# Kernel optimization log

Measured on AMD Instinct MI355X. Metric: run time of the kernel, lower is better.

Reference implementation:

```python
import jax, jax.numpy as jnp
import numpy as np

N = 10000
E = 160000
UNITS = 64
NUM_RBF = 32
CUTOFF = 1.0


def _xavier(k, shape):
    fan_out, fan_in = shape
    lim = float(np.sqrt(6.0 / (fan_in + fan_out)))
    return jax.random.uniform(k, shape, minval=-lim, maxval=lim, dtype=jnp.float32)


def setup_inputs() -> dict:
    key = jax.random.key(0)
    ks = jax.random.split(key, 16)
    inp = {
        "edge_index": jax.random.randint(ks[0], (2, E), 0, N),
        "edge_weight": jax.random.uniform(ks[1], (E,), dtype=jnp.float32),
        "edge_attr": jax.random.normal(ks[2], (E, NUM_RBF), dtype=jnp.float32),
        "X": jax.random.normal(ks[3], (N, UNITS, 3, 3), dtype=jnp.float32),
        # scalar MLP: num_rbf -> units -> 2*units -> 3*units
        "Ws0": _xavier(ks[4], (UNITS, NUM_RBF)), "bs0": jnp.zeros((UNITS,), jnp.float32),
        "Ws1": _xavier(ks[5], (2 * UNITS, UNITS)), "bs1": jnp.zeros((2 * UNITS,), jnp.float32),
        "Ws2": _xavier(ks[6], (3 * UNITS, 2 * UNITS)), "bs2": jnp.zeros((3 * UNITS,), jnp.float32),
    }
    for i in range(6):
        inp[f"Wt{i}"] = _xavier(ks[7 + i], (UNITS, UNITS))
    return inp


def cosine_cutoff(r, cutoff):
    return jnp.where(r < cutoff, 0.5 * (jnp.cos(jnp.pi * r / cutoff) + 1.0), 0.0)


def tensor_norm(X):
    # X: [N, units, 3, 3] -> [N, units]
    return jnp.sum(X * X, axis=(-2, -1))


def decompose_tensor(X):
    eye = jnp.eye(3, dtype=X.dtype)
    trace = jnp.trace(X, axis1=-2, axis2=-1)  # [N, units]
    I = (trace / 3.0)[..., None, None] * eye
    A = 0.5 * (X - jnp.swapaxes(X, -2, -1))
    S = 0.5 * (X + jnp.swapaxes(X, -2, -1)) - I
    return I, A, S


def channel_linear(T, W):
    # linear over the channel dim: [N, c, 3, 3] x [d, c] -> [N, d, 3, 3]
    return jnp.einsum('ncij,dc->ndij', T, W)


def reference(edge_index, edge_weight, edge_attr, X,
              Ws0, bs0, Ws1, bs1, Ws2, bs2,
              Wt0, Wt1, Wt2, Wt3, Wt4, Wt5):
    act = jax.nn.silu
    C = cosine_cutoff(edge_weight, CUTOFF)  # [E]
    h = act(edge_attr @ Ws0.T + bs0)
    h = act(h @ Ws1.T + bs1)
    h = act(h @ Ws2.T + bs2)  # [E, 3*units]
    ea = (h * C[:, None]).reshape(h.shape[0], UNITS, 3)  # [E, units, 3]

    X = X / (tensor_norm(X) + 1.0)[..., None, None]
    I, A, S = decompose_tensor(X)
    I = channel_linear(I, Wt0)
    A = channel_linear(A, Wt1)
    S = channel_linear(S, Wt2)
    Y = I + A + S

    src, dst = edge_index[0], edge_index[1]
    n = X.shape[0]
    # message = per-edge radial scaling of gathered node tensors; aggregate at src
    Im = jax.ops.segment_sum(ea[..., 0, None, None] * I[dst], src, num_segments=n)
    Am = jax.ops.segment_sum(ea[..., 1, None, None] * A[dst], src, num_segments=n)
    Sm = jax.ops.segment_sum(ea[..., 2, None, None] * S[dst], src, num_segments=n)
    msg = Im + Am + Sm

    # O(3): symmetrized product of batched 3x3 matmuls
    AB = jnp.matmul(msg, Y) + jnp.matmul(Y, msg)
    I2, A2, S2 = decompose_tensor(AB)
    normp1 = (tensor_norm(I2 + A2 + S2) + 1.0)[..., None, None]
    I2 = channel_linear(I2 / normp1, Wt3)
    A2 = channel_linear(A2 / normp1, Wt4)
    S2 = channel_linear(S2 / normp1, Wt5)
    dX = I2 + A2 + S2
    return X + dX + jnp.matmul(dX, dX)
```

## Files before the change

### kernel.cpp

```cpp
#include <hip/hip_runtime.h>
#include <math.h>

#define NN 10000
#define EE 160000

#define OFF_WTT 0
#define OFF_PK  24576
#define OFF_B2P 41984
#define OFF_IASH 42176
#define OFF_EAH 3242176
#define OFF_ATTRP 18602176
#define OFF_CP  21162176
#define OFF_INT 21322176

typedef __attribute__((ext_vector_type(8))) _Float16 h16x8;
typedef __attribute__((ext_vector_type(2))) __fp16 fp16x2_raw;
typedef __attribute__((ext_vector_type(4))) float f32x4;

__device__ __forceinline__ float silu_f(float x) {
    return x * __builtin_amdgcn_rcpf(1.0f + __expf(-x));
}
__device__ __forceinline__ unsigned int pkh(float a, float b) {
    union { fp16x2_raw h; unsigned int u; } cv;
    cv.h = __builtin_amdgcn_cvt_pkrtz(a, b);
    return cv.u;
}
__device__ __forceinline__ unsigned short f2h(float f) {
    union { _Float16 h; unsigned short u; } cv; cv.h = (_Float16)f; return cv.u;
}
__device__ __forceinline__ float h2f(unsigned short s) {
    union { unsigned short u; _Float16 h; } cv; cv.u = s; return (float)cv.h;
}
__device__ __forceinline__ float h2f_lo(unsigned int u) { return h2f((unsigned short)(u & 0xffffu)); }
__device__ __forceinline__ float h2f_hi(unsigned int u) { return h2f((unsigned short)(u >> 16)); }

__global__ void k_prep(const float* __restrict__ Wt0, const float* __restrict__ Wt1,
                       const float* __restrict__ Wt2, const float* __restrict__ Wt3,
                       const float* __restrict__ Wt4, const float* __restrict__ Wt5,
                       const float* __restrict__ Ws0, const float* __restrict__ Ws1,
                       const float* __restrict__ Ws2, const float* __restrict__ bs2,
                       const int* __restrict__ ei,
                       float* __restrict__ WtT, unsigned short* __restrict__ PK,
                       float* __restrict__ bs2p, int* __restrict__ counts) {
    int idx = blockIdx.x * 256 + threadIdx.x;
    if (idx < 24576) {
        int k = idx >> 12, r = idx & 4095;
        int c = r >> 6, d = r & 63;
        const float* W = (k == 0) ? Wt0 : (k == 1) ? Wt1 : (k == 2) ? Wt2
                       : (k == 3) ? Wt3 : (k == 4) ? Wt4 : Wt5;
        WtT[idx] = W[d * 64 + c];
    } else if (idx < 26624) {
        int q = idx - 24576;
        int ot = q >> 9, r = q & 511, lane = r >> 3, j = r & 7;
        int k = ((lane >> 4) * 8) + j, o = ot * 16 + (lane & 15);
        PK[q] = f2h(Ws0[o * 32 + k]);
    } else if (idx < 34816) {
        int q = idx - 24576;
        int i = q - 2048, ch = i >> 9, r = i & 511, lane = r >> 3, j = r & 7;
        int ot = ch >> 1, ks = ch & 1;
        int k = ks * 32 + (lane >> 4) * 8 + j, o = ot * 16 + (lane & 15);
        PK[q] = f2h(Ws1[o * 64 + k]);
    } else if (idx < 59392) {
        int q = idx - 24576;
        int i = q - 10240, ch = i >> 9, r = i & 511, lane = r >> 3, j = r & 7;
        int ot = ch >> 2, ks = ch & 3;
        int k = ks * 32 + (lane >> 4) * 8 + j;
        int op = ot * 16 + (lane & 15);
        int o = (op & 63) * 3 + (op >> 6);
        PK[q] = f2h(Ws2[o * 128 + k]);
    } else if (idx < 59584) {
        int op = idx - 59392;
        bs2p[op] = bs2[(op & 63) * 3 + (op >> 6)];
    } else if (idx < 59584 + EE) {
        int e = idx - 59584;
        atomicAdd(&counts[ei[e]], 1);
    }
}

__global__ __launch_bounds__(256) void k_scan(const int* __restrict__ counts,
                                              int* __restrict__ offsets) {
    __shared__ int sums[256];
    int t = threadIdx.x;
    int base = t * 40;
    int s = 0;
    if (base < NN) {
        const int4* p = (const int4*)(counts + base);
#pragma unroll
        for (int q = 0; q < 10; ++q) { int4 a = p[q]; s += a.x + a.y + a.z + a.w; }
    }
    sums[t] = s;
    __syncthreads();
    for (int off = 1; off < 256; off <<= 1) {
        int tmp = (t >= off) ? sums[t - off] : 0;
        __syncthreads();
        sums[t] += tmp;
        __syncthreads();
    }
    int run = sums[t] - s;
    if (base < NN) {
        const int4* p = (const int4*)(counts + base);
#pragma unroll
        for (int q = 0; q < 10; ++q) {
            int4 a = p[q];
            offsets[base + 4 * q + 0] = run; run += a.x;
            offsets[base + 4 * q + 1] = run; run += a.y;
            offsets[base + 4 * q + 2] = run; run += a.z;
            offsets[base + 4 * q + 3] = run; run += a.w;
        }
    }
    if (t == 255) offsets[NN] = run;
}

__global__ void k_fill(const int* __restrict__ ei, const int* __restrict__ offsets,
                       const float* __restrict__ attr, const float* __restrict__ ew,
                       int* __restrict__ cursor, int* __restrict__ dstp,
                       unsigned short* __restrict__ attrP, float* __restrict__ Cp) {
    int e = blockIdx.x * 256 + threadIdx.x;
    if (e < EE) {
        int s = ei[e];
        int pos = offsets[s] + atomicAdd(&cursor[s], 1);
        dstp[pos] = ei[EE + e];
        const float4* ap = (const float4*)(attr + (size_t)e * 32);
        unsigned int pk[16];
#pragma unroll
        for (int q = 0; q < 8; ++q) {
            float4 v = ap[q];
            pk[2 * q]     = pkh(v.x, v.y);
            pk[2 * q + 1] = pkh(v.z, v.w);
        }
        uint4* dst = (uint4*)(attrP + (size_t)pos * 32);
#pragma unroll
        for (int q = 0; q < 4; ++q)
            dst[q] = make_uint4(pk[4 * q], pk[4 * q + 1], pk[4 * q + 2], pk[4 * q + 3]);
        float rw = ew[e];
        Cp[pos] = (rw < 1.0f) ? 0.5f * (cosf(3.14159265358979f * rw) + 1.0f) : 0.0f;
    }
}

__global__ __launch_bounds__(256) void k_mlpnp(const unsigned short* __restrict__ attrP,
                                               const float* __restrict__ Cp,
                                               const unsigned short* __restrict__ PK,
                                               const float* __restrict__ bs0,
                                               const float* __restrict__ bs1,
                                               const float* __restrict__ bs2p,
                                               const float* __restrict__ X,
                                               const float* __restrict__ WtT,
                                               unsigned short* __restrict__ eah,
                                               unsigned int* __restrict__ IASu) {
    __shared__ unsigned short SH[4][4352];
    int t = threadIdx.x, w = t >> 6, l = t & 63;
    if (blockIdx.x < EE / 128) {
        int lr = l & 15, lg = l >> 4;
        int base = blockIdx.x * 128 + w * 32;
        unsigned short* Hh = SH[w];
        const h16x8* P1 = (const h16x8*)PK;
        const h16x8* P2 = (const h16x8*)(PK + 2048);
        const h16x8* P3 = (const h16x8*)(PK + 10240);
        union { h16x8 h; uint4 v; } B1[2];
        float C[2];
#pragma unroll
        for (int tt = 0; tt < 2; ++tt) {
            int p = base + tt * 16 + lr;
            B1[tt].v = *((const uint4*)(attrP + (size_t)p * 32) + lg);
            C[tt] = Cp[p];
        }
#pragma unroll
        for (int ot = 0; ot < 4; ++ot) {
            h16x8 wf = P1[ot * 64 + l];
            float4 bb = *(const float4*)&bs0[ot * 16 + lg * 4];
#pragma unroll
            for (int tt = 0; tt < 2; ++tt) {
                f32x4 acc = {bb.x, bb.y, bb.z, bb.w};
                acc = __builtin_amdgcn_mfma_f32_16x16x32_f16(wf, B1[tt].h, acc, 0, 0, 0);
                unsigned int u01 = pkh(silu_f(acc[0]), silu_f(acc[1]));
                unsigned int u23 = pkh(silu_f(acc[2]), silu_f(acc[3]));
                *(uint2*)&Hh[tt * 2176 + lr * 136 + ot * 16 + lg * 4] = make_uint2(u01, u23);
            }
        }
        __builtin_amdgcn_wave_barrier();
        h16x8 B2a[2], B2b[2];
#pragma unroll
        for (int tt = 0; tt < 2; ++tt) {
            B2a[tt] = *(const h16x8*)&Hh[tt * 2176 + lr * 136 + lg * 8];
            B2b[tt] = *(const h16x8*)&Hh[tt * 2176 + lr * 136 + 32 + lg * 8];
        }
        __builtin_amdgcn_wave_barrier();
#pragma unroll
        for (int ot = 0; ot < 8; ++ot) {
            h16x8 wf0 = P2[(ot * 2 + 0) * 64 + l];
            h16x8 wf1 = P2[(ot * 2 + 1) * 64 + l];
            float4 bb = *(const float4*)&bs1[ot * 16 + lg * 4];
#pragma unroll
            for (int tt = 0; tt < 2; ++tt) {
                f32x4 acc = {bb.x, bb.y, bb.z, bb.w};
                acc = __builtin_amdgcn_mfma_f32_16x16x32_f16(wf0, B2a[tt], acc, 0, 0, 0);
                acc = __builtin_amdgcn_mfma_f32_16x16x32_f16(wf1, B2b[tt], acc, 0, 0, 0);
                unsigned int u01 = pkh(silu_f(acc[0]), silu_f(acc[1]));
                unsigned int u23 = pkh(silu_f(acc[2]), silu_f(acc[3]));
                *(uint2*)&Hh[tt * 2176 + lr * 136 + ot * 16 + lg * 4] = make_uint2(u01, u23);
            }
        }
        __builtin_amdgcn_wave_barrier();
        h16x8 B3[4][2];
#pragma unroll
        for (int ks = 0; ks < 4; ++ks)
#pragma unroll
            for (int tt = 0; tt < 2; ++tt)
                B3[ks][tt] = *(const h16x8*)&Hh[tt * 2176 + lr * 136 + ks * 32 + lg * 8];
#pragma unroll
        for (int ot = 0; ot < 12; ++ot) {
            h16x8 wf0 = P3[(ot * 4 + 0) * 64 + l];
            h16x8 wf1 = P3[(ot * 4 + 1) * 64 + l];
            h16x8 wf2 = P3[(ot * 4 + 2) * 64 + l];
            h16x8 wf3 = P3[(ot * 4 + 3) * 64 + l];
            float4 bb = *(const float4*)&bs2p[ot * 16 + lg * 4];
#pragma unroll
            for (int tt = 0; tt < 2; ++tt) {
                f32x4 acc = {bb.x, bb.y, bb.z, bb.w};
                acc = __builtin_amdgcn_mfma_f32_16x16x32_f16(wf0, B3[0][tt], acc, 0, 0, 0);
                acc = __builtin_amdgcn_mfma_f32_16x16x32_f16(wf1, B3[1][tt], acc, 0, 0, 0);
                acc = __builtin_amdgcn_mfma_f32_16x16x32_f16(wf2, B3[2][tt], acc, 0, 0, 0);
                acc = __builtin_amdgcn_mfma_f32_16x16x32_f16(wf3, B3[3][tt], acc, 0, 0, 0);
                unsigned int u01 = pkh(silu_f(acc[0]) * C[tt], silu_f(acc[1]) * C[tt]);
                unsigned int u23 = pkh(silu_f(acc[2]) * C[tt], silu_f(acc[3]) * C[tt]);
                *(uint2*)&eah[(size_t)(base + tt * 16 + lr) * 192 + ot * 16 + lg * 4]
                    = make_uint2(u01, u23);
            }
        }
    } else {
        int c = l;
        int n = (blockIdx.x - EE / 128) * 4 + w;
        float* xs = (float*)SH[w];
        float (*L12)[12] = (float (*)[12])(xs + 576);
#pragma unroll
        for (int i = 0; i < 9; i++) xs[c + 64 * i] = X[(size_t)n * 576 + c + 64 * i];
        __builtin_amdgcn_wave_barrier();
        float x[9];
#pragma unroll
        for (int j = 0; j < 9; j++) x[j] = xs[c * 9 + j];
        float nrm = 0.f;
#pragma unroll
        for (int j = 0; j < 9; j++) nrm += x[j] * x[j];
        float inv = __builtin_amdgcn_rcpf(nrm + 1.0f);
#pragma unroll
        for (int j = 0; j < 9; j++) x[j] *= inv;
        float tr3 = (x[0] + x[4] + x[8]) * (1.0f / 3.0f);
        L12[c][0] = tr3;
        L12[c][1] = 0.5f * (x[1] - x[3]);
        L12[c][2] = 0.5f * (x[2] - x[6]);
        L12[c][3] = 0.5f * (x[5] - x[7]);
        L12[c][4] = x[0] - tr3;
        L12[c][5] = x[4] - tr3;
        L12[c][6] = 0.5f * (x[1] + x[3]);
        L12[c][7] = 0.5f * (x[2] + x[6]);
        L12[c][8] = 0.5f * (x[5] + x[7]);
        __builtin_amdgcn_wave_barrier();
        int d = c;
        const float* W0 = WtT;
        const float* W1 = WtT + 4096;
        const float* W2 = WtT + 8192;
        float aI = 0, aA0 = 0, aA1 = 0, aA2 = 0, aS0 = 0, aS1 = 0, aS2 = 0, aS3 = 0, aS4 = 0;
        for (int cc = 0; cc < 64; ++cc) {
            float w0 = W0[cc * 64 + d], w1 = W1[cc * 64 + d], w2 = W2[cc * 64 + d];
            float4 L0 = *(const float4*)&L12[cc][0];
            float4 L1 = *(const float4*)&L12[cc][4];
            float L8 = L12[cc][8];
            aI  += w0 * L0.x;
            aA0 += w1 * L0.y; aA1 += w1 * L0.z; aA2 += w1 * L0.w;
            aS0 += w2 * L1.x; aS1 += w2 * L1.y; aS2 += w2 * L1.z;
            aS3 += w2 * L1.w; aS4 += w2 * L8;
        }
        unsigned int* op = IASu + (size_t)n * 320 + d;
        op[0]   = pkh(aI, aA0);
        op[64]  = pkh(aA1, aA2);
        op[128] = pkh(aS0, aS1);
        op[192] = pkh(aS2, aS3);
        op[256] = pkh(aS4, 0.0f);
    }
}

__global__ __launch_bounds__(256) void k_aggout(const int* __restrict__ offsets,
                                                const int* __restrict__ dstp,
                                                const unsigned short* __restrict__ eah,
                                                const unsigned int* __restrict__ IASu,
                                                const float* __restrict__ X,
                                                const float* __restrict__ WtT,
                                                float* __restrict__ out) {
    int t = threadIdx.x, w = t >> 6, c = t & 63;
    int n = blockIdx.x * 4 + w;
    __shared__ float XS[4][576];
    __shared__ float LO[4][768];
    float* xs = XS[w];
    float* lo = LO[w];
#pragma unroll
    for (int i = 0; i < 9; i++) xs[c + 64 * i] = X[(size_t)n * 576 + c + 64 * i];

    int beg = offsets[n], end = offsets[n + 1];
    float m0 = 0, m1 = 0, m2 = 0, m3 = 0, m4 = 0, m5 = 0, m6 = 0, m7 = 0, m8 = 0;
    int i = beg;
    for (; i + 4 <= end; i += 4) {
        float a[4][3];
        unsigned int u[4][5];
#pragma unroll
        for (int q = 0; q < 4; ++q) {
            const unsigned short* ep = eah + (size_t)(i + q) * 192;
            a[q][0] = h2f(ep[c]); a[q][1] = h2f(ep[64 + c]); a[q][2] = h2f(ep[128 + c]);
            const unsigned int* p = IASu + (size_t)dstp[i + q] * 320 + c;
            u[q][0] = p[0]; u[q][1] = p[64]; u[q][2] = p[128]; u[q][3] = p[192]; u[q][4] = p[256];
        }
#pragma unroll
        for (int q = 0; q < 4; ++q) {
            m0 += a[q][0] * h2f_lo(u[q][0]); m1 += a[q][1] * h2f_hi(u[q][0]);
            m2 += a[q][1] * h2f_lo(u[q][1]); m3 += a[q][1] * h2f_hi(u[q][1]);
            m4 += a[q][2] * h2f_lo(u[q][2]); m5 += a[q][2] * h2f_hi(u[q][2]);
            m6 += a[q][2] * h2f_lo(u[q][3]); m7 += a[q][2] * h2f_hi(u[q][3]);
            m8 += a[q][2] * h2f_lo(u[q][4]);
        }
    }
    for (; i < end; ++i) {
        const unsigned short* ep = eah + (size_t)i * 192;
        float a0 = h2f(ep[c]), a1 = h2f(ep[64 + c]), a2 = h2f(ep[128 + c]);
        const unsigned int* p = IASu + (size_t)dstp[i] * 320 + c;
        unsigned int u0 = p[0], u1 = p[64], u2 = p[128], u3 = p[192], u4 = p[256];
        m0 += a0 * h2f_lo(u0); m1 += a1 * h2f_hi(u0);
        m2 += a1 * h2f_lo(u1); m3 += a1 * h2f_hi(u1);
        m4 += a2 * h2f_lo(u2); m5 += a2 * h2f_hi(u2);
        m6 += a2 * h2f_lo(u3); m7 += a2 * h2f_hi(u3);
        m8 += a2 * h2f_lo(u4);
    }
    const unsigned int* yp = IASu + (size_t)n * 320 + c;
    unsigned int y0 = yp[0], y1 = yp[64], y2 = yp[128], y3 = yp[192], y4 = yp[256];
    float yI = h2f_lo(y0), yA0 = h2f_hi(y0), yA1 = h2f_lo(y1), yA2 = h2f_hi(y1);
    float yS0 = h2f_lo(y2), yS1 = h2f_hi(y2), yS2 = h2f_lo(y3), yS3 = h2f_hi(y3);
    float yS4 = h2f_lo(y4);

    float M[3][3] = {
        { m0 + m4,   m1 + m6,  m2 + m7 },
        { -m1 + m6,  m0 + m5,  m3 + m8 },
        { -m2 + m7, -m3 + m8,  m0 - m4 - m5 } };
    float Y[3][3] = {
        { yI + yS0,   yA0 + yS2,  yA1 + yS3 },
        { -yA0 + yS2, yI + yS1,   yA2 + yS4 },
        { -yA1 + yS3, -yA2 + yS4, yI - yS0 - yS1 } };
    float AB[3][3];
#pragma unroll
    for (int ii = 0; ii < 3; ii++)
#pragma unroll
        for (int j = 0; j < 3; j++) {
            float s = 0.f;
#pragma unroll
            for (int k = 0; k < 3; k++) s += M[ii][k] * Y[k][j] + Y[ii][k] * M[k][j];
            AB[ii][j] = s;
        }
    float tr3 = (AB[0][0] + AB[1][1] + AB[2][2]) * (1.0f / 3.0f);
    float fro = 0.f;
#pragma unroll
    for (int ii = 0; ii < 3; ii++)
#pragma unroll
        for (int j = 0; j < 3; j++) fro += AB[ii][j] * AB[ii][j];
    float inv = __builtin_amdgcn_rcpf(fro + 1.0f);
    float (*L12)[12] = (float (*)[12])lo;
    L12[c][0] = tr3 * inv;
    L12[c][1] = 0.5f * (AB[0][1] - AB[1][0]) * inv;
    L12[c][2] = 0.5f * (AB[0][2] - AB[2][0]) * inv;
    L12[c][3] = 0.5f * (AB[1][2] - AB[2][1]) * inv;
    L12[c][4] = (AB[0][0] - tr3) * inv;
    L12[c][5] = (AB[1][1] - tr3) * inv;
    L12[c][6] = 0.5f * (AB[0][1] + AB[1][0]) * inv;
    L12[c][7] = 0.5f * (AB[0][2] + AB[2][0]) * inv;
    L12[c][8] = 0.5f * (AB[1][2] + AB[2][1]) * inv;
    __builtin_amdgcn_wave_barrier();
    int d = c;
    const float* W3 = WtT + 3 * 4096;
    const float* W4 = WtT + 4 * 4096;
    const float* W5 = WtT + 5 * 4096;
    float aI = 0, aA0 = 0, aA1 = 0, aA2 = 0, aS0 = 0, aS1 = 0, aS2 = 0, aS3 = 0, aS4 = 0;
    for (int cc = 0; cc < 64; ++cc) {
        float w3 = W3[cc * 64 + d], w4 = W4[cc * 64 + d], w5 = W5[cc * 64 + d];
        float4 L0 = *(const float4*)&L12[cc][0];
        float4 L1 = *(const float4*)&L12[cc][4];
        float L8 = L12[cc][8];
        aI  += w3 * L0.x;
        aA0 += w4 * L0.y; aA1 += w4 * L0.z; aA2 += w4 * L0.w;
        aS0 += w5 * L1.x; aS1 += w5 * L1.y; aS2 += w5 * L1.z;
        aS3 += w5 * L1.w; aS4 += w5 * L8;
    }
    float dX[3][3] = {
        { aI + aS0,   aA0 + aS2,  aA1 + aS3 },
        { -aA0 + aS2, aI + aS1,   aA2 + aS4 },
        { -aA1 + aS3, -aA2 + aS4, aI - aS0 - aS1 } };
    float D2[3][3];
#pragma unroll
    for (int ii = 0; ii < 3; ii++)
#pragma unroll
        for (int j = 0; j < 3; j++) {
            float s = 0.f;
#pragma unroll
            for (int k = 0; k < 3; k++) s += dX[ii][k] * dX[k][j];
            D2[ii][j] = s;
        }
    float x[9];
    __builtin_amdgcn_wave_barrier();
#pragma unroll
    for (int j = 0; j < 9; j++) x[j] = xs[d * 9 + j];
    float nrm = 0.f;
#pragma unroll
    for (int j = 0; j < 9; j++) nrm += x[j] * x[j];
    float xinv = __builtin_amdgcn_rcpf(nrm + 1.0f);
    __builtin_amdgcn_wave_barrier();
#pragma unroll
    for (int ii = 0; ii < 3; ii++)
#pragma unroll
        for (int j = 0; j < 3; j++)
            lo[d * 9 + ii * 3 + j] = x[ii * 3 + j] * xinv + dX[ii][j] + D2[ii][j];
    __builtin_amdgcn_wave_barrier();
#pragma unroll
    for (int ii = 0; ii < 9; ii++) out[(size_t)n * 576 + c + 64 * ii] = lo[c + 64 * ii];
}

extern "C" void kernel_launch(void* const* d_in, const int* in_sizes, int n_in,
                              void* d_out, int out_size, void* d_ws, size_t ws_size,
                              hipStream_t stream) {
    (void)in_sizes; (void)n_in; (void)out_size; (void)ws_size;
    const int* ei = (const int*)d_in[0];
    const float* ew = (const float*)d_in[1];
    const float* attr = (const float*)d_in[2];
    const float* X = (const float*)d_in[3];
    const float* Ws0 = (const float*)d_in[4];
    const float* bs0 = (const float*)d_in[5];
    const float* Ws1 = (const float*)d_in[6];
    const float* bs1 = (const float*)d_in[7];
    const float* Ws2 = (const float*)d_in[8];
    const float* bs2 = (const float*)d_in[9];
    const float* Wt0 = (const float*)d_in[10];
    const float* Wt1 = (const float*)d_in[11];
    const float* Wt2 = (const float*)d_in[12];
    const float* Wt3 = (const float*)d_in[13];
    const float* Wt4 = (const float*)d_in[14];
    const float* Wt5 = (const float*)d_in[15];
    float* ws = (float*)d_ws;
    int* ibase = (int*)(ws + OFF_INT);
    int* counts = ibase;
    int* cursor = ibase + NN;
    int* offsets = ibase + 2 * NN;
    int* dstp = ibase + 3 * NN + 1;
    unsigned short* PK = (unsigned short*)(ws + OFF_PK);
    unsigned int* IASu = (unsigned int*)(ws + OFF_IASH);
    unsigned short* eah = (unsigned short*)(ws + OFF_EAH);
    unsigned short* attrP = (unsigned short*)(ws + OFF_ATTRP);
    float* Cp = ws + OFF_CP;

    (void)hipMemsetAsync(counts, 0, 2 * NN * sizeof(int), stream);
    k_prep<<<(59584 + EE + 255) / 256, 256, 0, stream>>>(
        Wt0, Wt1, Wt2, Wt3, Wt4, Wt5, Ws0, Ws1, Ws2, bs2, ei,
        ws, PK, ws + OFF_B2P, counts);
    k_scan<<<1, 256, 0, stream>>>(counts, offsets);
    k_fill<<<(EE + 255) / 256, 256, 0, stream>>>(ei, offsets, attr, ew, cursor, dstp, attrP, Cp);
    k_mlpnp<<<EE / 128 + NN / 4, 256, 0, stream>>>(attrP, Cp, PK, bs0, bs1, ws + OFF_B2P,
                                                   X, ws, eah, IASu);
    k_aggout<<<NN / 4, 256, 0, stream>>>(offsets, dstp, eah, IASu, X, ws, (float*)d_out);
}
```

Baseline: 150.3 us.

## Split fused MLP/node kernel and pass MLP activations via ds_bpermute instead of LDS

The combined edge-MLP and node-prep kernel is split into two launches: k_nodeprep for the per-node decomposition and channel linear, and k_mlp for the edge MLP. k_mlp now handles 16 edges per wave instead of 32 and drops the shared staging buffer. Hidden activations are rearranged between MFMA layers with cross-lane ds_bpermute shuffles and selects. This removes LDS use and pressure from the MLP so more waves can be resident, at the cost of an extra kernel launch, more permute instructions, and weight fragments reloaded per 16-edge tile instead of per 32-edge tile.

```diff
diff --git a/kernel.cpp b/kernel.cpp
--- a/kernel.cpp
+++ b/kernel.cpp
@@ -33,6 +33,9 @@
 }
 __device__ __forceinline__ float h2f_lo(unsigned int u) { return h2f((unsigned short)(u & 0xffffu)); }
 __device__ __forceinline__ float h2f_hi(unsigned int u) { return h2f((unsigned short)(u >> 16)); }
+__device__ __forceinline__ unsigned int bperm(int addr, unsigned int v) {
+    return (unsigned int)__builtin_amdgcn_ds_bpermute(addr, (int)v);
+}
 
 __global__ void k_prep(const float* __restrict__ Wt0, const float* __restrict__ Wt1,
                        const float* __restrict__ Wt2, const float* __restrict__ Wt3,
@@ -137,145 +140,132 @@
     }
 }
 
-__global__ __launch_bounds__(256) void k_mlpnp(const unsigned short* __restrict__ attrP,
-                                               const float* __restrict__ Cp,
-                                               const unsigned short* __restrict__ PK,
-                                               const float* __restrict__ bs0,
-                                               const float* __restrict__ bs1,
-                                               const float* __restrict__ bs2p,
-                                               const float* __restrict__ X,
-                                               const float* __restrict__ WtT,
-                                               unsigned short* __restrict__ eah,
-                                               unsigned int* __restrict__ IASu) {
-    __shared__ unsigned short SH[4][4352];
+__global__ __launch_bounds__(256) void k_nodeprep(const float* __restrict__ X,
+                                                  const float* __restrict__ WtT,
+                                                  unsigned int* __restrict__ IASu) {
+    int t = threadIdx.x, w = t >> 6, c = t & 63;
+    int n = blockIdx.x * 4 + w;
+    __shared__ float XS[4][576];
+    __shared__ float L[4][64][12];
+    float* xs = XS[w];
+#pragma unroll
+    for (int i = 0; i < 9; i++) xs[c + 64 * i] = X[(size_t)n * 576 + c + 64 * i];
+    __builtin_amdgcn_wave_barrier();
+    float x[9];
+#pragma unroll
+    for (int j = 0; j < 9; j++) x[j] = xs[c * 9 + j];
+    float nrm = 0.f;
+#pragma unroll
+    for (int j = 0; j < 9; j++) nrm += x[j] * x[j];
+    float inv = __builtin_amdgcn_rcpf(nrm + 1.0f);
+#pragma unroll
+    for (int j = 0; j < 9; j++) x[j] *= inv;
+    float tr3 = (x[0] + x[4] + x[8]) * (1.0f / 3.0f);
+    L[w][c][0] = tr3;
+    L[w][c][1] = 0.5f * (x[1] - x[3]);
+    L[w][c][2] = 0.5f * (x[2] - x[6]);
+    L[w][c][3] = 0.5f * (x[5] - x[7]);
+    L[w][c][4] = x[0] - tr3;
+    L[w][c][5] = x[4] - tr3;
+    L[w][c][6] = 0.5f * (x[1] + x[3]);
+    L[w][c][7] = 0.5f * (x[2] + x[6]);
+    L[w][c][8] = 0.5f * (x[5] + x[7]);
+    __builtin_amdgcn_wave_barrier();
+    int d = c;
+    const float* W0 = WtT;
+    const float* W1 = WtT + 4096;
+    const float* W2 = WtT + 8192;
+    float aI = 0, aA0 = 0, aA1 = 0, aA2 = 0, aS0 = 0, aS1 = 0, aS2 = 0, aS3 = 0, aS4 = 0;
+    for (int cc = 0; cc < 64; ++cc) {
+        float w0 = W0[cc * 64 + d], w1 = W1[cc * 64 + d], w2 = W2[cc * 64 + d];
+        float4 L0 = *(const float4*)&L[w][cc][0];
+        float4 L1 = *(const float4*)&L[w][cc][4];
+        float L8 = L[w][cc][8];
+        aI  += w0 * L0.x;
+        aA0 += w1 * L0.y; aA1 += w1 * L0.z; aA2 += w1 * L0.w;
+        aS0 += w2 * L1.x; aS1 += w2 * L1.y; aS2 += w2 * L1.z;
+        aS3 += w2 * L1.w; aS4 += w2 * L8;
+    }
+    unsigned int* op = IASu + (size_t)n * 320 + d;
+    op[0]   = pkh(aI, aA0);
+    op[64]  = pkh(aA1, aA2);
+    op[128] = pkh(aS0, aS1);
+    op[192] = pkh(aS2, aS3);
+    op[256] = pkh(aS4, 0.0f);
+}
+
+__global__ __launch_bounds__(256) void k_mlp(const unsigned short* __restrict__ attrP,
+                                             const float* __restrict__ Cp,
+                                             const unsigned short* __restrict__ PK,
+                                             const float* __restrict__ bs0,
+                                             const float* __restrict__ bs1,
+                                             const float* __restrict__ bs2p,
+                                             unsigned short* __restrict__ eah) {
     int t = threadIdx.x, w = t >> 6, l = t & 63;
-    if (blockIdx.x < EE / 128) {
-        int lr = l & 15, lg = l >> 4;
-        int base = blockIdx.x * 128 + w * 32;
-        unsigned short* Hh = SH[w];
-        const h16x8* P1 = (const h16x8*)PK;
-        const h16x8* P2 = (const h16x8*)(PK + 2048);
-        const h16x8* P3 = (const h16x8*)(PK + 10240);
-        union { h16x8 h; uint4 v; } B1[2];
-        float C[2];
-#pragma unroll
-        for (int tt = 0; tt < 2; ++tt) {
-            int p = base + tt * 16 + lr;
-            B1[tt].v = *((const uint4*)(attrP + (size_t)p * 32) + lg);
-            C[tt] = Cp[p];
-        }
-#pragma unroll
-        for (int ot = 0; ot < 4; ++ot) {
-            h16x8 wf = P1[ot * 64 + l];
-            float4 bb = *(const float4*)&bs0[ot * 16 + lg * 4];
-#pragma unroll
-            for (int tt = 0; tt < 2; ++tt) {
-                f32x4 acc = {bb.x, bb.y, bb.z, bb.w};
-                acc = __builtin_amdgcn_mfma_f32_16x16x32_f16(wf, B1[tt].h, acc, 0, 0, 0);
-                unsigned int u01 = pkh(silu_f(acc[0]), silu_f(acc[1]));
-                unsigned int u23 = pkh(silu_f(acc[2]), silu_f(acc[3]));
-                *(uint2*)&Hh[tt * 2176 + lr * 136 + ot * 16 + lg * 4] = make_uint2(u01, u23);
-            }
-        }
-        __builtin_amdgcn_wave_barrier();
-        h16x8 B2a[2], B2b[2];
-#pragma unroll
-        for (int tt = 0; tt < 2; ++tt) {
-            B2a[tt] = *(const h16x8*)&Hh[tt * 2176 + lr * 136 + lg * 8];
-            B2b[tt] = *(const h16x8*)&Hh[tt * 2176 + lr * 136 + 32 + lg * 8];
-        }
-        __builtin_amdgcn_wave_barrier();
-#pragma unroll
-        for (int ot = 0; ot < 8; ++ot) {
-            h16x8 wf0 = P2[(ot * 2 + 0) * 64 + l];
-            h16x8 wf1 = P2[(ot * 2 + 1) * 64 + l];
-            float4 bb = *(const float4*)&bs1[ot * 16 + lg * 4];
-#pragma unroll
-            for (int tt = 0; tt < 2; ++tt) {
-                f32x4 acc = {bb.x, bb.y, bb.z, bb.w};
-                acc = __builtin_amdgcn_mfma_f32_16x16x32_f16(wf0, B2a[tt], acc, 0, 0, 0);
-                acc = __builtin_amdgcn_mfma_f32_16x16x32_f16(wf1, B2b[tt], acc, 0, 0, 0);
-                unsigned int u01 = pkh(silu_f(acc[0]), silu_f(acc[1]));
-                unsigned int u23 = pkh(silu_f(acc[2]), silu_f(acc[3]));
-                *(uint2*)&Hh[tt * 2176 + lr * 136 + ot * 16 + lg * 4] = make_uint2(u01, u23);
-            }
-        }
-        __builtin_amdgcn_wave_barrier();
-        h16x8 B3[4][2];
-#pragma unroll
-        for (int ks = 0; ks < 4; ++ks)
-#pragma unroll
-            for (int tt = 0; tt < 2; ++tt)
-                B3[ks][tt] = *(const h16x8*)&Hh[tt * 2176 + lr * 136 + ks * 32 + lg * 8];
-#pragma unroll
-        for (int ot = 0; ot < 12; ++ot) {
-            h16x8 wf0 = P3[(ot * 4 + 0) * 64 + l];
-            h16x8 wf1 = P3[(ot * 4 + 1) * 64 + l];
-            h16x8 wf2 = P3[(ot * 4 + 2) * 64 + l];
-            h16x8 wf3 = P3[(ot * 4 + 3) * 64 + l];
-            float4 bb = *(const float4*)&bs2p[ot * 16 + lg * 4];
-#pragma unroll
-            for (int tt = 0; tt < 2; ++tt) {
-                f32x4 acc = {bb.x, bb.y, bb.z, bb.w};
-                acc = __builtin_amdgcn_mfma_f32_16x16x32_f16(wf0, B3[0][tt], acc, 0, 0, 0);
-                acc = __builtin_amdgcn_mfma_f32_16x16x32_f16(wf1, B3[1][tt], acc, 0, 0, 0);
-                acc = __builtin_amdgcn_mfma_f32_16x16x32_f16(wf2, B3[2][tt], acc, 0, 0, 0);
-                acc = __builtin_amdgcn_mfma_f32_16x16x32_f16(wf3, B3[3][tt], acc, 0, 0, 0);
-                unsigned int u01 = pkh(silu_f(acc[0]) * C[tt], silu_f(acc[1]) * C[tt]);
-                unsigned int u23 = pkh(silu_f(acc[2]) * C[tt], silu_f(acc[3]) * C[tt]);
-                *(uint2*)&eah[(size_t)(base + tt * 16 + lr) * 192 + ot * 16 + lg * 4]
-                    = make_uint2(u01, u23);
-            }
-        }
-    } else {
-        int c = l;
-        int n = (blockIdx.x - EE / 128) * 4 + w;
-        float* xs = (float*)SH[w];
-        float (*L12)[12] = (float (*)[12])(xs + 576);
-#pragma unroll
-        for (int i = 0; i < 9; i++) xs[c + 64 * i] = X[(size_t)n * 576 + c + 64 * i];
-        __builtin_amdgcn_wave_barrier();
-        float x[9];
-#pragma unroll
-        for (int j = 0; j < 9; j++) x[j] = xs[c * 9 + j];
-        float nrm = 0.f;
-#pragma unroll
-        for (int j = 0; j < 9; j++) nrm += x[j] * x[j];
-        float inv = __builtin_amdgcn_rcpf(nrm + 1.0f);
-#pragma unroll
-        for (int j = 0; j < 9; j++) x[j] *= inv;
-        float tr3 = (x[0] + x[4] + x[8]) * (1.0f / 3.0f);
-        L12[c][0] = tr3;
-        L12[c][1] = 0.5f * (x[1] - x[3]);
-        L12[c][2] = 0.5f * (x[2] - x[6]);
-        L12[c][3] = 0.5f * (x[5] - x[7]);
-        L12[c][4] = x[0] - tr3;
-        L12[c][5] = x[4] - tr3;
-        L12[c][6] = 0.5f * (x[1] + x[3]);
-        L12[c][7] = 0.5f * (x[2] + x[6]);
-        L12[c][8] = 0.5f * (x[5] + x[7]);
-        __builtin_amdgcn_wave_barrier();
-        int d = c;
-        const float* W0 = WtT;
-        const float* W1 = WtT + 4096;
-        const float* W2 = WtT + 8192;
-        float aI = 0, aA0 = 0, aA1 = 0, aA2 = 0, aS0 = 0, aS1 = 0, aS2 = 0, aS3 = 0, aS4 = 0;
-        for (int cc = 0; cc < 64; ++cc) {
-            float w0 = W0[cc * 64 + d], w1 = W1[cc * 64 + d], w2 = W2[cc * 64 + d];
-            float4 L0 = *(const float4*)&L12[cc][0];
-            float4 L1 = *(const float4*)&L12[cc][4];
-            float L8 = L12[cc][8];
-            aI  += w0 * L0.x;
-            aA0 += w1 * L0.y; aA1 += w1 * L0.z; aA2 += w1 * L0.w;
-            aS0 += w2 * L1.x; aS1 += w2 * L1.y; aS2 += w2 * L1.z;
-            aS3 += w2 * L1.w; aS4 += w2 * L8;
-        }
-        unsigned int* op = IASu + (size_t)n * 320 + d;
-        op[0]   = pkh(aI, aA0);
-        op[64]  = pkh(aA1, aA2);
-        op[128] = pkh(aS0, aS1);
-        op[192] = pkh(aS2, aS3);
-        op[256] = pkh(aS4, 0.0f);
+    int e = l & 15, lg = l >> 4;
+    int pos = blockIdx.x * 64 + w * 16 + e;
+    const h16x8* P1 = (const h16x8*)PK;
+    const h16x8* P2 = (const h16x8*)(PK + 2048);
+    const h16x8* P3 = (const h16x8*)(PK + 10240);
+    union U8 { h16x8 h; unsigned int u[4]; uint4 v; };
+    U8 B1;
+    B1.v = *((const uint4*)(attrP + (size_t)pos * 32) + lg);
+    float C = Cp[pos];
+    int src0 = ((lg & 1) * 32 + e) * 4;
+    int src1 = src0 + 64;
+    bool hi = (lg >= 2);
+
+    unsigned int h01[8], h23[8];
+#pragma unroll
+    for (int ot = 0; ot < 4; ++ot) {
+        float4 bb = *(const float4*)&bs0[ot * 16 + lg * 4];
+        f32x4 acc = {bb.x, bb.y, bb.z, bb.w};
+        acc = __builtin_amdgcn_mfma_f32_16x16x32_f16(P1[ot * 64 + l], B1.h, acc, 0, 0, 0);
+        h01[ot] = pkh(silu_f(acc[0]), silu_f(acc[1]));
+        h23[ot] = pkh(silu_f(acc[2]), silu_f(acc[3]));
+    }
+    U8 B2a, B2b;
+    {
+        unsigned int a, b;
+        a = bperm(src0, h01[0]); b = bperm(src0, h01[1]); B2a.u[0] = hi ? b : a;
+        a = bperm(src0, h23[0]); b = bperm(src0, h23[1]); B2a.u[1] = hi ? b : a;
+        a = bperm(src1, h01[0]); b = bperm(src1, h01[1]); B2a.u[2] = hi ? b : a;
+        a = bperm(src1, h23[0]); b = bperm(src1, h23[1]); B2a.u[3] = hi ? b : a;
+        a = bperm(src0, h01[2]); b = bperm(src0, h01[3]); B2b.u[0] = hi ? b : a;
+        a = bperm(src0, h23[2]); b = bperm(src0, h23[3]); B2b.u[1] = hi ? b : a;
+        a = bperm(src1, h01[2]); b = bperm(src1, h01[3]); B2b.u[2] = hi ? b : a;
+        a = bperm(src1, h23[2]); b = bperm(src1, h23[3]); B2b.u[3] = hi ? b : a;
+    }
+#pragma unroll
+    for (int ot = 0; ot < 8; ++ot) {
+        float4 bb = *(const float4*)&bs1[ot * 16 + lg * 4];
+        f32x4 acc = {bb.x, bb.y, bb.z, bb.w};
+        acc = __builtin_amdgcn_mfma_f32_16x16x32_f16(P2[(ot * 2 + 0) * 64 + l], B2a.h, acc, 0, 0, 0);
+        acc = __builtin_amdgcn_mfma_f32_16x16x32_f16(P2[(ot * 2 + 1) * 64 + l], B2b.h, acc, 0, 0, 0);
+        h01[ot] = pkh(silu_f(acc[0]), silu_f(acc[1]));
+        h23[ot] = pkh(silu_f(acc[2]), silu_f(acc[3]));
+    }
+    U8 B3[4];
+#pragma unroll
+    for (int ks = 0; ks < 4; ++ks) {
+        unsigned int a, b;
+        a = bperm(src0, h01[ks * 2]); b = bperm(src0, h01[ks * 2 + 1]); B3[ks].u[0] = hi ? b : a;
+        a = bperm(src0, h23[ks * 2]); b = bperm(src0, h23[ks * 2 + 1]); B3[ks].u[1] = hi ? b : a;
+        a = bperm(src1, h01[ks * 2]); b = bperm(src1, h01[ks * 2 + 1]); B3[ks].u[2] = hi ? b : a;
+        a = bperm(src1, h23[ks * 2]); b = bperm(src1, h23[ks * 2 + 1]); B3[ks].u[3] = hi ? b : a;
+    }
+    size_t ebase = (size_t)pos * 192;
+#pragma unroll
+    for (int ot = 0; ot < 12; ++ot) {
+        float4 bb = *(const float4*)&bs2p[ot * 16 + lg * 4];
+        f32x4 acc = {bb.x, bb.y, bb.z, bb.w};
+        acc = __builtin_amdgcn_mfma_f32_16x16x32_f16(P3[(ot * 4 + 0) * 64 + l], B3[0].h, acc, 0, 0, 0);
+        acc = __builtin_amdgcn_mfma_f32_16x16x32_f16(P3[(ot * 4 + 1) * 64 + l], B3[1].h, acc, 0, 0, 0);
+        acc = __builtin_amdgcn_mfma_f32_16x16x32_f16(P3[(ot * 4 + 2) * 64 + l], B3[2].h, acc, 0, 0, 0);
+        acc = __builtin_amdgcn_mfma_f32_16x16x32_f16(P3[(ot * 4 + 3) * 64 + l], B3[3].h, acc, 0, 0, 0);
+        unsigned int u01 = pkh(silu_f(acc[0]) * C, silu_f(acc[1]) * C);
+        unsigned int u23 = pkh(silu_f(acc[2]) * C, silu_f(acc[3]) * C);
+        *(uint2*)&eah[ebase + ot * 16 + lg * 4] = make_uint2(u01, u23);
     }
 }
 
@@ -456,7 +446,7 @@
         ws, PK, ws + OFF_B2P, counts);
     k_scan<<<1, 256, 0, stream>>>(counts, offsets);
     k_fill<<<(EE + 255) / 256, 256, 0, stream>>>(ei, offsets, attr, ew, cursor, dstp, attrP, Cp);
-    k_mlpnp<<<EE / 128 + NN / 4, 256, 0, stream>>>(attrP, Cp, PK, bs0, bs1, ws + OFF_B2P,
-                                                   X, ws, eah, IASu);
+    k_nodeprep<<<NN / 4, 256, 0, stream>>>(X, ws, IASu);
+    k_mlp<<<EE / 64, 256, 0, stream>>>(attrP, Cp, PK, bs0, bs1, ws + OFF_B2P, eah);
     k_aggout<<<NN / 4, 256, 0, stream>>>(offsets, dstp, eah, IASu, X, ws, (float*)d_out);
 }
```

After: 160.0 us. 1.06x slower.
